# Optimization experiments

Hardware: AMD Instinct MI355X
Metric: run time of the kernel (lower is better)

The kernel has to match this reference:

```python
import jax, jax.numpy as jnp
import numpy as np

DIM = 256
D_STATE = 64
D_CONV = 4
EXPAND = 2
D_INNER = EXPAND * DIM  # 512
DT_RANK = (DIM + 15) // 16  # 16
BS, N1, N2 = 4, 64, 64


def setup_inputs() -> dict:
    key = jax.random.key(0)
    ks = jax.random.split(key, 12)
    s = 0.02
    x = jax.random.normal(ks[0], (BS, N1, N2, DIM), jnp.float32)
    W_in = jax.random.normal(ks[1], (2 * D_INNER, DIM), jnp.float32) * s
    conv_w = jax.random.normal(ks[2], (D_INNER, D_CONV), jnp.float32) * s
    conv_b = jax.random.normal(ks[3], (D_INNER,), jnp.float32) * s
    W_x = jax.random.normal(ks[4], (DT_RANK + 2 * D_STATE, D_INNER), jnp.float32) * s
    W_dt = jax.random.normal(ks[5], (D_INNER, DT_RANK), jnp.float32) * s
    b_dt = jax.random.normal(ks[6], (D_INNER,), jnp.float32) * s - 4.0  # softplus -> small dt
    A_log = jnp.log(jnp.broadcast_to(jnp.arange(1, D_STATE + 1, dtype=jnp.float32), (D_INNER, D_STATE)))
    D_param = jnp.ones((D_INNER,), jnp.float32)
    W_out = jax.random.normal(ks[7], (DIM, D_INNER), jnp.float32) * s
    ln1_w = jnp.ones((DIM,), jnp.float32)
    ln1_b = jnp.zeros((DIM,), jnp.float32)
    ln2_w = jnp.ones((DIM,), jnp.float32)
    ln2_b = jnp.zeros((DIM,), jnp.float32)
    return dict(x=x, ln1_w=ln1_w, ln1_b=ln1_b, ln2_w=ln2_w, ln2_b=ln2_b,
                W_in=W_in, conv_w=conv_w, conv_b=conv_b, W_x=W_x,
                W_dt=W_dt, b_dt=b_dt, A_log=A_log, D_param=D_param, W_out=W_out)


def _layernorm(x, w, b, eps=1e-6):
    mu = jnp.mean(x, axis=-1, keepdims=True)
    var = jnp.mean((x - mu) ** 2, axis=-1, keepdims=True)
    return (x - mu) * jax.lax.rsqrt(var + eps) * w + b


def _silu(x):
    return x * jax.nn.sigmoid(x)


def _selective_scan(u, dt, A, B, C, D):
    # u, dt: (Bt, L, di); B, C: (Bt, L, ds); A: (di, ds); D: (di,)
    Bt, L, di = u.shape
    ds = A.shape[1]

    def step(h, inp):
        u_t, dt_t, B_t, C_t = inp  # (Bt,di),(Bt,di),(Bt,ds),(Bt,ds)
        dA = jnp.exp(dt_t[:, :, None] * A)                       # (Bt, di, ds)
        h = dA * h + (dt_t * u_t)[:, :, None] * B_t[:, None, :]  # (Bt, di, ds)
        y_t = jnp.einsum('bds,bs->bd', h, C_t)
        return h, y_t

    h0 = jnp.zeros((Bt, di, ds), u.dtype)
    xs = (u.transpose(1, 0, 2), dt.transpose(1, 0, 2),
          B.transpose(1, 0, 2), C.transpose(1, 0, 2))
    _, ys = jax.lax.scan(step, h0, xs)                           # (L, Bt, di)
    return ys.transpose(1, 0, 2) + u * D


def _mamba(xm, W_in, conv_w, conv_b, W_x, W_dt, b_dt, A_log, D_param, W_out):
    # xm: (Bt, L, d_model)
    xz = jnp.einsum('bld,ed->ble', xm, W_in)       # (Bt, L, 2*di)
    xc, z = jnp.split(xz, 2, axis=-1)
    # depthwise causal conv along L
    xc = xc.transpose(0, 2, 1)                     # (Bt, di, L)
    xc = jax.lax.conv_general_dilated(
        xc, conv_w[:, None, :], window_strides=(1,),
        padding=[(D_CONV - 1, 0)], feature_group_count=D_INNER,
        dimension_numbers=('NCH', 'OIH', 'NCH'))
    xc = _silu(xc + conv_b[None, :, None]).transpose(0, 2, 1)  # (Bt, L, di)
    x_dbl = jnp.einsum('bld,ed->ble', xc, W_x)     # (Bt, L, dt_rank+2*ds)
    dt, Bm, Cm = jnp.split(x_dbl, [DT_RANK, DT_RANK + D_STATE], axis=-1)
    dt = jax.nn.softplus(jnp.einsum('blr,dr->bld', dt, W_dt) + b_dt)  # (Bt, L, di)
    A = -jnp.exp(A_log)                            # (di, ds)
    y = _selective_scan(xc, dt, A, Bm, Cm, D_param)
    y = y * _silu(z)
    return jnp.einsum('bld,od->blo', y, W_out)     # (Bt, L, d_model)


def reference(x, ln1_w, ln1_b, ln2_w, ln2_b, W_in, conv_w, conv_b, W_x,
              W_dt, b_dt, A_log, D_param, W_out):
    bs, n1, n2, d = x.shape
    x_norm = _layernorm(x, ln1_w, ln1_b)
    x1 = x_norm.reshape(bs, n1 * n2, d)                                  # row-major
    x2 = x_norm.transpose(0, 2, 1, 3).reshape(bs, n1 * n2, d)            # column-major
    xm = jnp.concatenate([x1, x2], axis=0)                               # (2*bs, L, d)
    xm = _mamba(xm, W_in, conv_w, conv_b, W_x, W_dt, b_dt, A_log, D_param, W_out)
    y = _layernorm(xm, ln2_w, ln2_b)
    y1, y2 = y[:bs], y[bs:]
    y1 = y1.reshape(bs, n1, n2, d)
    y2 = y2.reshape(bs, n2, n1, d).transpose(0, 2, 1, 3)
    return x + y1 + y2
```

## Files before the change

### kernel.cpp

```cpp
#include <hip/hip_runtime.h>
#include <hip/hip_bf16.h>

typedef unsigned short ushort_t;
typedef unsigned int uint_t;
typedef __attribute__((ext_vector_type(8))) short short8;
typedef __attribute__((ext_vector_type(4))) float f32x4;

#define DIMC 256
#define D_INNER 512
#define D_STATE 64
#define DT_RANK 16
#define LSEQ 4096
#define BS2 8
#define MROWS (BS2*LSEQ)

__device__ __forceinline__ float b2f(ushort_t u) {
    union { uint_t i; float f; } v; v.i = ((uint_t)u) << 16; return v.f;
}
__device__ __forceinline__ ushort_t f2b(float f) {
    union { float f; uint_t i; } v; v.f = f;
    uint_t r = v.i + 0x7FFFu + ((v.i >> 16) & 1u);
    return (ushort_t)(r >> 16);
}

typedef __attribute__((address_space(1))) const unsigned int gas_u32;
typedef __attribute__((address_space(3))) unsigned int las_u32;
__device__ __forceinline__ void gload16(const void* g, void* l) {
    __builtin_amdgcn_global_load_lds((gas_u32*)g, (las_u32*)l, 16, 0, 0);
}

__global__ void cvtw3(const float* __restrict__ s0, ushort_t* __restrict__ d0,
                      const float* __restrict__ s1, ushort_t* __restrict__ d1,
                      const float* __restrict__ s2, ushort_t* __restrict__ d2) {
    int i = blockIdx.x * 256 + threadIdx.x;
    const int n0 = 1024 * 256, n1 = 144 * 512, n2 = 256 * 512;
    if (i < n0) d0[i] = f2b(s0[i]);
    else if (i < n0 + n1) d1[i - n0] = f2b(s1[i - n0]);
    else if (i < n0 + n1 + n2) d2[i - n0 - n1] = f2b(s2[i - n0 - n1]);
}

__global__ void ln1_build_xm(const float* __restrict__ x,
                             const float* __restrict__ w,
                             const float* __restrict__ bb,
                             ushort_t* __restrict__ xm) {
    int row = blockIdx.x;
    int c = threadIdx.x;
    float v = x[(size_t)row * DIMC + c];
    float s1 = v, s2 = v * v;
    for (int off = 32; off; off >>= 1) {
        s1 += __shfl_xor(s1, off, 64);
        s2 += __shfl_xor(s2, off, 64);
    }
    __shared__ float sa[4], sb[4];
    int widx = c >> 6, lane = c & 63;
    if (lane == 0) { sa[widx] = s1; sb[widx] = s2; }
    __syncthreads();
    s1 = sa[0] + sa[1] + sa[2] + sa[3];
    s2 = sb[0] + sb[1] + sb[2] + sb[3];
    float mu = s1 * (1.0f / 256.0f);
    float var = s2 * (1.0f / 256.0f) - mu * mu;
    float xn = (v - mu) * rsqrtf(var + 1e-6f) * w[c] + bb[c];
    ushort_t o = f2b(xn);
    int b = row >> 12, l = row & 4095, i = l >> 6, j = l & 63;
    xm[((size_t)b * LSEQ + l) * DIMC + c] = o;
    xm[((size_t)(4 + b) * LSEQ + (j * 64 + i)) * DIMC + c] = o;
}

__global__ void __launch_bounds__(256, 4)
gemm128(const ushort_t* __restrict__ A,
        const ushort_t* __restrict__ W,
        ushort_t* __restrict__ C, int M, int N, int K) {
    __shared__ ushort_t Ash[128 * 32];
    __shared__ ushort_t Bsh[128 * 32];
    int tid = threadIdx.x;
    int lane = tid & 63, widx = tid >> 6;
    int wm = widx & 1, wn = widx >> 1;
    int l16 = lane & 15, quad = lane >> 4;
    int mblk = blockIdx.x * 128, nblk = blockIdx.y * 128;
    f32x4 acc[4][4];
    #pragma unroll
    for (int i = 0; i < 4; ++i)
        #pragma unroll
        for (int j = 0; j < 4; ++j)
            acc[i][j] = f32x4{0.0f, 0.0f, 0.0f, 0.0f};
    int srow = tid >> 2;
    int sseg = (tid & 3) * 8;
    bool jv[4];
    #pragma unroll
    for (int j = 0; j < 4; ++j) jv[j] = (nblk + wn * 64 + j * 16) < N;

    for (int k0 = 0; k0 < K; k0 += 32) {
        __syncthreads();
        #pragma unroll
        for (int q = 0; q < 2; ++q) {
            int row = q * 64 + srow;
            gload16(&A[(size_t)(mblk + row) * K + k0 + sseg], &Ash[row * 32 + sseg]);
            gload16(&W[(size_t)(nblk + row) * K + k0 + sseg], &Bsh[row * 32 + sseg]);
        }
        __syncthreads();
        short8 af[4], bf[4];
        #pragma unroll
        for (int i = 0; i < 4; ++i)
            af[i] = *(const short8*)&Ash[(wm * 64 + i * 16 + l16) * 32 + quad * 8];
        #pragma unroll
        for (int j = 0; j < 4; ++j)
            bf[j] = *(const short8*)&Bsh[(wn * 64 + j * 16 + l16) * 32 + quad * 8];
        #pragma unroll
        for (int i = 0; i < 4; ++i)
            #pragma unroll
            for (int j = 0; j < 4; ++j)
                if (jv[j])
                    acc[i][j] = __builtin_amdgcn_mfma_f32_16x16x32_bf16(af[i], bf[j], acc[i][j], 0, 0, 0);
    }
    #pragma unroll
    for (int i = 0; i < 4; ++i) {
        #pragma unroll
        for (int j = 0; j < 4; ++j) {
            if (!jv[j]) continue;
            int col = nblk + wn * 64 + j * 16 + l16;
            #pragma unroll
            for (int r = 0; r < 4; ++r) {
                int row = mblk + wm * 64 + i * 16 + quad * 4 + r;
                C[(size_t)row * N + col] = f2b(acc[i][j][r]);
            }
        }
    }
}

__global__ void __launch_bounds__(256, 4)
gemm128_split(const ushort_t* __restrict__ A,
              const ushort_t* __restrict__ W,
              ushort_t* __restrict__ outX,
              ushort_t* __restrict__ outZ) {
    const int K = 256;
    __shared__ ushort_t Ash[128 * 32];
    __shared__ ushort_t Bsh[128 * 32];
    int tid = threadIdx.x;
    int lane = tid & 63, widx = tid >> 6;
    int wm = widx & 1, wn = widx >> 1;
    int l16 = lane & 15, quad = lane >> 4;
    int mblk = blockIdx.x * 128, nblk = blockIdx.y * 128;
    f32x4 acc[4][4];
    #pragma unroll
    for (int i = 0; i < 4; ++i)
        #pragma unroll
        for (int j = 0; j < 4; ++j)
            acc[i][j] = f32x4{0.0f, 0.0f, 0.0f, 0.0f};
    int srow = tid >> 2;
    int sseg = (tid & 3) * 8;
    for (int k0 = 0; k0 < K; k0 += 32) {
        __syncthreads();
        #pragma unroll
        for (int q = 0; q < 2; ++q) {
            int row = q * 64 + srow;
            gload16(&A[(size_t)(mblk + row) * K + k0 + sseg], &Ash[row * 32 + sseg]);
            gload16(&W[(size_t)(nblk + row) * K + k0 + sseg], &Bsh[row * 32 + sseg]);
        }
        __syncthreads();
        short8 af[4], bf[4];
        #pragma unroll
        for (int i = 0; i < 4; ++i)
            af[i] = *(const short8*)&Ash[(wm * 64 + i * 16 + l16) * 32 + quad * 8];
        #pragma unroll
        for (int j = 0; j < 4; ++j)
            bf[j] = *(const short8*)&Bsh[(wn * 64 + j * 16 + l16) * 32 + quad * 8];
        #pragma unroll
        for (int i = 0; i < 4; ++i)
            #pragma unroll
            for (int j = 0; j < 4; ++j)
                acc[i][j] = __builtin_amdgcn_mfma_f32_16x16x32_bf16(af[i], bf[j], acc[i][j], 0, 0, 0);
    }
    #pragma unroll
    for (int i = 0; i < 4; ++i) {
        #pragma unroll
        for (int j = 0; j < 4; ++j) {
            int colg = nblk + wn * 64 + j * 16 + l16;
            ushort_t* dst = (colg < 512) ? outX : outZ;
            int col = colg & 511;
            #pragma unroll
            for (int r = 0; r < 4; ++r) {
                int row = mblk + wm * 64 + i * 16 + quad * 4 + r;
                dst[(size_t)row * 512 + col] = f2b(acc[i][j][r]);
            }
        }
    }
}

__global__ void conv_silu_t(const ushort_t* __restrict__ xh,
                            const float* __restrict__ cw,
                            const float* __restrict__ cb,
                            ushort_t* __restrict__ xc,
                            ushort_t* __restrict__ u_T) {
    int bt0 = blockIdx.x * 64;
    int d0  = blockIdx.y * 64;
    int b   = bt0 >> 12;
    int t0  = bt0 & 4095;
    __shared__ ushort_t tin[67][66];
    __shared__ ushort_t tout[64][66];
    int tid = threadIdx.x, lane = tid & 63, widx = tid >> 6;
    for (int r = widx; r < 67; r += 4) {
        int tt = t0 - 3 + r;
        tin[r][lane] = (tt >= 0) ? xh[((size_t)bt0 - 3 + r) * 512 + d0 + lane] : (ushort_t)0;
    }
    __syncthreads();
    for (int dd = widx; dd < 64; dd += 4) {
        int d = d0 + dd;
        float acc = cb[d];
        #pragma unroll
        for (int k = 0; k < 4; ++k)
            acc += cw[d * 4 + k] * b2f(tin[lane + k][dd]);
        float s = acc / (1.0f + __expf(-acc));
        ushort_t o = f2b(s);
        u_T[((size_t)b * 512 + d) * 4096 + t0 + lane] = o;
        tout[lane][dd] = o;
    }
    __syncthreads();
    for (int r = widx; r < 64; r += 4)
        xc[((size_t)bt0 + r) * 512 + d0 + lane] = tout[r][lane];
}

__global__ void dt_sp_t(const ushort_t* __restrict__ xdbl,
                        const float* __restrict__ wdt,
                        const float* __restrict__ bdt,
                        const ushort_t* __restrict__ u_T,
                        ushort_t* __restrict__ dt_T,
                        ushort_t* __restrict__ w_T,
                        float2* __restrict__ BCf) {
    int bt0 = blockIdx.x * 64;
    int d0  = blockIdx.y * 64;
    int b   = bt0 >> 12;
    int t0  = bt0 & 4095;
    __shared__ float din[64][17];
    int tid = threadIdx.x;
    for (int i = tid; i < 64 * 16; i += 256) {
        int r = i >> 4, k = i & 15;
        din[r][k] = b2f(xdbl[((size_t)bt0 + r) * 144 + k]);
    }
    __syncthreads();
    int lane = tid & 63, widx = tid >> 6;
    for (int dd = widx; dd < 64; dd += 4) {
        int d = d0 + dd;
        float acc = bdt[d];
        #pragma unroll
        for (int k = 0; k < 16; ++k)
            acc += din[lane][k] * wdt[d * 16 + k];
        float sp = (acc > 20.0f) ? acc : log1pf(__expf(acc));
        size_t idx = ((size_t)b * 512 + d) * 4096 + t0 + lane;
        dt_T[idx] = f2b(sp);
        float uvv = b2f(u_T[idx]);
        w_T[idx] = f2b(sp * uvv);
    }
    if (blockIdx.y == 0) {
        for (int i = tid; i < 64 * 64; i += 256) {
            size_t row = (size_t)bt0 + (i >> 6);
            int s = i & 63;
            const ushort_t* rp = xdbl + row * 144;
            BCf[(row << 6) + s] = make_float2(b2f(rp[16 + s]), b2f(rp[80 + s]));
        }
    }
}

template<int LVL>
__device__ __forceinline__ float merge_lvl_t(float left, float right, int lane) {
    bool bit = (lane >> LVL) & 1;
    float send = bit ? left : right;
    float keep = bit ? right : left;
    float recv;
    if constexpr (LVL == 0)
        recv = __int_as_float(__builtin_amdgcn_update_dpp(
            0, __float_as_int(send), 0xB1, 0xF, 0xF, false));
    else if constexpr (LVL == 1)
        recv = __int_as_float(__builtin_amdgcn_update_dpp(
            0, __float_as_int(send), 0x4E, 0xF, 0xF, false));
    else
        recv = __shfl_xor(send, 1 << LVL, 64);
    return keep + recv;
}

__global__ void __launch_bounds__(256, 4)
scan10(const ushort_t* __restrict__ dt_T,
       ushort_t* uT_ysT,
       const ushort_t* __restrict__ w_T,
       const float2* __restrict__ BCf,
       const float* __restrict__ Alog,
       const float* __restrict__ Dp) {
    __shared__ float2 BCsh[64][64];
    int tid = threadIdx.x;
    int lane = tid & 63, widx = tid >> 6;
    int wid = blockIdx.x * 4 + widx;
    int b = wid >> 9, d = wid & 511;
    float a2 = -__expf(Alog[d * 64 + lane]) * 1.442695041f;
    float Dd = Dp[d];
    float h = 0.0f;
    size_t rowT = ((size_t)b * 512 + d) * 4096;
    uint_t rowTu = __builtin_amdgcn_readfirstlane((uint_t)rowT);
    size_t base = (size_t)b * LSEQ;
    for (int t0 = 0; t0 < LSEQ; t0 += 64) {
        __syncthreads();
        {
            const char* gsrc = (const char*)(BCf + (((size_t)(base + t0)) << 6));
            char* ldst = (char*)&BCsh[0][0];
            size_t woff = (size_t)widx * 8192;
            #pragma unroll
            for (int it = 0; it < 8; ++it) {
                size_t o = woff + (size_t)it * 1024 + (size_t)lane * 16;
                gload16(gsrc + o, ldst + o);
            }
        }
        const uint_t* dtw = (const uint_t*)(dt_T + rowTu) + (t0 >> 1);
        const uint_t* wwp = (const uint_t*)(w_T + rowTu) + (t0 >> 1);
        float uv = b2f(uT_ysT[rowT + t0 + lane]);
        __syncthreads();
        float acc[4], s4, s5, yfin = 0.0f, v16 = 0.0f;
        #pragma unroll 1
        for (int j1 = 0; j1 < 4; ++j1) {
            #pragma unroll
            for (int jj = 0; jj < 16; ++jj) {
                int j = j1 * 16 + jj;
                uint_t pd = dtw[j >> 1];
                uint_t pw = wwp[j >> 1];
                float sdt = __uint_as_float((jj & 1) ? (pd & 0xFFFF0000u) : (pd << 16));
                float sw  = __uint_as_float((jj & 1) ? (pw & 0xFFFF0000u) : (pw << 16));
                float2 bc = BCsh[j][lane];
                float dA = __builtin_amdgcn_exp2f(sdt * a2);
                float Bw = sw * bc.x;
                h = dA * h + Bw;
                float v = h * bc.y;
                const int dest = (jj == 15) ? 4 : __builtin_ctz(~(unsigned)jj);
                if (0 < dest) v = merge_lvl_t<0>(acc[0], v, lane);
                if (1 < dest) v = merge_lvl_t<1>(acc[1], v, lane);
                if (2 < dest) v = merge_lvl_t<2>(acc[2], v, lane);
                if (3 < dest) v = merge_lvl_t<3>(acc[3], v, lane);
                if (jj == 15) v16 = v;
                else acc[dest] = v;
            }
            if ((j1 & 1) == 0) {
                s4 = v16;
            } else {
                float m = merge_lvl_t<4>(s4, v16, lane);
                if (j1 == 1) s5 = m;
                else yfin = merge_lvl_t<5>(s5, m, lane);
            }
        }
        float y = yfin + uv * Dd;
        uT_ysT[rowT + t0 + lane] = f2b(y);
    }
}

__global__ void gate_t(const ushort_t* __restrict__ ysT,
                       const ushort_t* __restrict__ zb,
                       ushort_t* __restrict__ ys) {
    int bt0 = blockIdx.x * 64;
    int d0  = blockIdx.y * 64;
    int b   = bt0 >> 12;
    int t0  = bt0 & 4095;
    __shared__ ushort_t tile[64][66];
    int tid = threadIdx.x, lane = tid & 63, widx = tid >> 6;
    for (int dd = widx; dd < 64; dd += 4)
        tile[dd][lane] = ysT[((size_t)b * 512 + d0 + dd) * 4096 + t0 + lane];
    __syncthreads();
    for (int r = widx; r < 64; r += 4) {
        float zv = b2f(zb[((size_t)bt0 + r) * 512 + d0 + lane]);
        float yv = b2f(tile[lane][r]);
        float g = zv / (1.0f + __expf(-zv));
        ys[((size_t)bt0 + r) * 512 + d0 + lane] = f2b(yv * g);
    }
}

__global__ void final_ln_add(const ushort_t* __restrict__ outm,
                             const float* __restrict__ x,
                             const float* __restrict__ w,
                             const float* __restrict__ bb,
                             float* __restrict__ out) {
    int row = blockIdx.x;
    int c = threadIdx.x;
    int b = row >> 12, l = row & 4095, i = l >> 6, j = l & 63;
    size_t rA = ((size_t)b * LSEQ + l) * DIMC;
    size_t rB = ((size_t)(4 + b) * LSEQ + (j * 64 + i)) * DIMC;
    float va = b2f(outm[rA + c]);
    float vb = b2f(outm[rB + c]);
    float s1 = va, s2 = va * va, s3 = vb, s4 = vb * vb;
    for (int off = 32; off; off >>= 1) {
        s1 += __shfl_xor(s1, off, 64);
        s2 += __shfl_xor(s2, off, 64);
        s3 += __shfl_xor(s3, off, 64);
        s4 += __shfl_xor(s4, off, 64);
    }
    __shared__ float sm[4][4];
    int widx = c >> 6, lane = c & 63;
    if (lane == 0) { sm[widx][0] = s1; sm[widx][1] = s2; sm[widx][2] = s3; sm[widx][3] = s4; }
    __syncthreads();
    s1 = sm[0][0] + sm[1][0] + sm[2][0] + sm[3][0];
    s2 = sm[0][1] + sm[1][1] + sm[2][1] + sm[3][1];
    s3 = sm[0][2] + sm[1][2] + sm[2][2] + sm[3][2];
    s4 = sm[0][3] + sm[1][3] + sm[2][3] + sm[3][3];
    float muA = s1 * (1.0f / 256.0f), varA = s2 * (1.0f / 256.0f) - muA * muA;
    float muB = s3 * (1.0f / 256.0f), varB = s4 * (1.0f / 256.0f) - muB * muB;
    float lw = w[c], lb = bb[c];
    float ya = (va - muA) * rsqrtf(varA + 1e-6f) * lw + lb;
    float yb = (vb - muB) * rsqrtf(varB + 1e-6f) * lw + lb;
    float xo = x[(size_t)row * DIMC + c];
    out[(size_t)row * DIMC + c] = xo + ya + yb;
}

extern "C" void kernel_launch(void* const* d_in, const int* in_sizes, int n_in,
                              void* d_out, int out_size, void* d_ws, size_t ws_size,
                              hipStream_t stream) {
    const float* x      = (const float*)d_in[0];
    const float* ln1_w  = (const float*)d_in[1];
    const float* ln1_b  = (const float*)d_in[2];
    const float* ln2_w  = (const float*)d_in[3];
    const float* ln2_b  = (const float*)d_in[4];
    const float* W_in   = (const float*)d_in[5];
    const float* conv_w = (const float*)d_in[6];
    const float* conv_b = (const float*)d_in[7];
    const float* W_x    = (const float*)d_in[8];
    const float* W_dt   = (const float*)d_in[9];
    const float* b_dt   = (const float*)d_in[10];
    const float* A_log  = (const float*)d_in[11];
    const float* D_par  = (const float*)d_in[12];
    const float* W_out  = (const float*)d_in[13];
    float* out = (float*)d_out;

    char* ws = (char*)d_ws;
    size_t off = 0;
    ushort_t* wb_in  = (ushort_t*)(ws + off); off += (size_t)1024 * 256 * 2;
    ushort_t* wb_x   = (ushort_t*)(ws + off); off += (size_t)144 * 512 * 2;
    ushort_t* wb_out = (ushort_t*)(ws + off); off += (size_t)256 * 512 * 2;
    const size_t R0 = (size_t)MROWS * DIMC * 2;
    const size_t R1 = (size_t)MROWS * 512 * 2;
    ushort_t* r0 = (ushort_t*)(ws + off); off += R0;
    ushort_t* r1 = (ushort_t*)(ws + off); off += R1;
    ushort_t* r2 = (ushort_t*)(ws + off); off += R1;
    ushort_t* r3 = (ushort_t*)(ws + off); off += R1;
    ushort_t* r4 = (ushort_t*)(ws + off); off += R1;
    float2*   BCf = (float2*)(ws + off);  off += (size_t)MROWS * 64 * 8;

    ushort_t* xm    = r0;
    ushort_t* xdbl  = r0;
    ushort_t* outm  = r0;
    ushort_t* xhalf = r1;
    ushort_t* dt_T  = r1;
    ushort_t* zb    = r2;
    ushort_t* xc    = r3;
    ushort_t* w_T   = r3;
    ushort_t* ys    = r3;
    ushort_t* u_T   = r4;

    const int ncvt = 1024 * 256 + 144 * 512 + 256 * 512;
    hipLaunchKernelGGL(cvtw3, dim3((ncvt + 255) / 256), dim3(256), 0, stream,
                       W_in, wb_in, W_x, wb_x, W_out, wb_out);

    hipLaunchKernelGGL(ln1_build_xm, dim3(4 * LSEQ), dim3(256), 0, stream,
                       x, ln1_w, ln1_b, xm);
    hipLaunchKernelGGL(gemm128_split, dim3(MROWS / 128, 8), dim3(256), 0, stream,
                       xm, wb_in, xhalf, zb);
    hipLaunchKernelGGL(conv_silu_t, dim3(MROWS / 64, 8), dim3(256), 0, stream,
                       xhalf, conv_w, conv_b, xc, u_T);
    hipLaunchKernelGGL(gemm128, dim3(MROWS / 128, 2), dim3(256), 0, stream,
                       xc, wb_x, xdbl, MROWS, 144, 512);
    hipLaunchKernelGGL(dt_sp_t, dim3(MROWS / 64, 8), dim3(256), 0, stream,
                       xdbl, W_dt, b_dt, u_T, dt_T, w_T, BCf);
    hipLaunchKernelGGL(scan10, dim3(BS2 * 512 / 4), dim3(256), 0, stream,
                       dt_T, u_T, w_T, BCf, A_log, D_par);
    hipLaunchKernelGGL(gate_t, dim3(MROWS / 64, 8), dim3(256), 0, stream,
                       u_T, zb, ys);
    hipLaunchKernelGGL(gemm128, dim3(MROWS / 128, 2), dim3(256), 0, stream,
                       ys, wb_out, outm, MROWS, 256, 512);
    hipLaunchKernelGGL(final_ln_add, dim3(4 * LSEQ), dim3(256), 0, stream,
                       outm, x, ln2_w, ln2_b, out);
}
```

Baseline: 730.4 us.

## Double-buffer BC staging in scan and use DPP-add and permlane swap merges

The scan kernel now stages B/C coefficients in 32-step halves into a two-slot LDS buffer, so the global-to-LDS load for the next half overlaps compute on the current half. This replaces the old load-then-barrier pattern that stalled every 64 steps. The lane-reduction merges are also cheaper: levels 0-1 use a fused v_add_f32_dpp in inline asm, and levels 4-5 use v_permlane16/32_swap instead of cross-lane shuffles. The output store is deferred by one iteration. In exchange it adds more barriers per iteration and inline asm with hand-placed s_nop hazards, which could be fragile.

```diff
diff --git a/kernel.cpp b/kernel.cpp
--- a/kernel.cpp
+++ b/kernel.cpp
@@ -265,26 +265,38 @@
     bool bit = (lane >> LVL) & 1;
     float send = bit ? left : right;
     float keep = bit ? right : left;
-    float recv;
-    if constexpr (LVL == 0)
-        recv = __int_as_float(__builtin_amdgcn_update_dpp(
-            0, __float_as_int(send), 0xB1, 0xF, 0xF, false));
-    else if constexpr (LVL == 1)
-        recv = __int_as_float(__builtin_amdgcn_update_dpp(
-            0, __float_as_int(send), 0x4E, 0xF, 0xF, false));
-    else
-        recv = __shfl_xor(send, 1 << LVL, 64);
-    return keep + recv;
+    float out;
+    if constexpr (LVL == 0) {
+        asm volatile("s_nop 1\n\t"
+                     "v_add_f32_dpp %0, %1, %2 quad_perm:[1,0,3,2] row_mask:0xf bank_mask:0xf"
+                     : "=v"(out) : "v"(send), "v"(keep));
+    } else if constexpr (LVL == 1) {
+        asm volatile("s_nop 1\n\t"
+                     "v_add_f32_dpp %0, %1, %2 quad_perm:[2,3,0,1] row_mask:0xf bank_mask:0xf"
+                     : "=v"(out) : "v"(send), "v"(keep));
+    } else {
+        float recv = __shfl_xor(send, 1 << LVL, 64);
+        out = keep + recv;
+    }
+    return out;
+}
+__device__ __forceinline__ float merge16_swap(float a, float b) {
+    asm volatile("s_nop 1\n\tv_permlane16_swap_b32 %0, %1" : "+v"(a), "+v"(b));
+    return a + b;
+}
+__device__ __forceinline__ float merge32_swap(float a, float b) {
+    asm volatile("s_nop 1\n\tv_permlane32_swap_b32 %0, %1" : "+v"(a), "+v"(b));
+    return a + b;
 }
 
 __global__ void __launch_bounds__(256, 4)
-scan10(const ushort_t* __restrict__ dt_T,
+scan11(const ushort_t* __restrict__ dt_T,
        ushort_t* uT_ysT,
        const ushort_t* __restrict__ w_T,
        const float2* __restrict__ BCf,
        const float* __restrict__ Alog,
        const float* __restrict__ Dp) {
-    __shared__ float2 BCsh[64][64];
+    __shared__ float2 BCsh[2][32][64];
     int tid = threadIdx.x;
     int lane = tid & 63, widx = tid >> 6;
     int wid = blockIdx.x * 4 + widx;
@@ -295,56 +307,65 @@
     size_t rowT = ((size_t)b * 512 + d) * 4096;
     uint_t rowTu = __builtin_amdgcn_readfirstlane((uint_t)rowT);
     size_t base = (size_t)b * LSEQ;
-    for (int t0 = 0; t0 < LSEQ; t0 += 64) {
-        __syncthreads();
-        {
-            const char* gsrc = (const char*)(BCf + (((size_t)(base + t0)) << 6));
-            char* ldst = (char*)&BCsh[0][0];
-            size_t woff = (size_t)widx * 8192;
-            #pragma unroll
-            for (int it = 0; it < 8; ++it) {
-                size_t o = woff + (size_t)it * 1024 + (size_t)lane * 16;
-                gload16(gsrc + o, ldst + o);
-            }
-        }
-        const uint_t* dtw = (const uint_t*)(dt_T + rowTu) + (t0 >> 1);
-        const uint_t* wwp = (const uint_t*)(w_T + rowTu) + (t0 >> 1);
-        float uv = b2f(uT_ysT[rowT + t0 + lane]);
-        __syncthreads();
-        float acc[4], s4, s5, yfin = 0.0f, v16 = 0.0f;
-        #pragma unroll 1
-        for (int j1 = 0; j1 < 4; ++j1) {
-            #pragma unroll
-            for (int jj = 0; jj < 16; ++jj) {
-                int j = j1 * 16 + jj;
-                uint_t pd = dtw[j >> 1];
-                uint_t pw = wwp[j >> 1];
-                float sdt = __uint_as_float((jj & 1) ? (pd & 0xFFFF0000u) : (pd << 16));
-                float sw  = __uint_as_float((jj & 1) ? (pw & 0xFFFF0000u) : (pw << 16));
-                float2 bc = BCsh[j][lane];
-                float dA = __builtin_amdgcn_exp2f(sdt * a2);
-                float Bw = sw * bc.x;
-                h = dA * h + Bw;
-                float v = h * bc.y;
-                const int dest = (jj == 15) ? 4 : __builtin_ctz(~(unsigned)jj);
-                if (0 < dest) v = merge_lvl_t<0>(acc[0], v, lane);
-                if (1 < dest) v = merge_lvl_t<1>(acc[1], v, lane);
-                if (2 < dest) v = merge_lvl_t<2>(acc[2], v, lane);
-                if (3 < dest) v = merge_lvl_t<3>(acc[3], v, lane);
-                if (jj == 15) v16 = v;
-                else acc[dest] = v;
-            }
-            if ((j1 & 1) == 0) {
-                s4 = v16;
-            } else {
-                float m = merge_lvl_t<4>(s4, v16, lane);
-                if (j1 == 1) s5 = m;
-                else yfin = merge_lvl_t<5>(s5, m, lane);
-            }
-        }
-        float y = yfin + uv * Dd;
-        uT_ysT[rowT + t0 + lane] = f2b(y);
-    }
+    const uint_t* dtw = (const uint_t*)(dt_T + rowTu);
+    const uint_t* wwp = (const uint_t*)(w_T + rowTu);
+
+    auto STAGE = [&](int bufi, int hs) {
+        const char* gsrc = (const char*)(BCf + (((size_t)(base + hs * 32)) << 6));
+        char* ldst = (char*)&BCsh[bufi][0][0];
+        size_t woff = (size_t)widx * 4096;
+        #pragma unroll
+        for (int it = 0; it < 4; ++it) {
+            size_t o = woff + (size_t)it * 1024 + (size_t)lane * 16;
+            gload16(gsrc + o, ldst + o);
+        }
+    };
+
+    float acc[4];
+    auto STEP16 = [&](int bufi, int jbase, int dwb) -> float {
+        float v16 = 0.0f;
+        #pragma unroll
+        for (int jj = 0; jj < 16; ++jj) {
+            uint_t pd = dtw[dwb + (jj >> 1)];
+            uint_t pw = wwp[dwb + (jj >> 1)];
+            float sdt = __uint_as_float((jj & 1) ? (pd & 0xFFFF0000u) : (pd << 16));
+            float sw  = __uint_as_float((jj & 1) ? (pw & 0xFFFF0000u) : (pw << 16));
+            float2 bc = BCsh[bufi][jbase + jj][lane];
+            float dA = __builtin_amdgcn_exp2f(sdt * a2);
+            h = dA * h + sw * bc.x;
+            float v = h * bc.y;
+            const int dest = (jj == 15) ? 4 : __builtin_ctz(~(unsigned)jj);
+            if (0 < dest) v = merge_lvl_t<0>(acc[0], v, lane);
+            if (1 < dest) v = merge_lvl_t<1>(acc[1], v, lane);
+            if (2 < dest) v = merge_lvl_t<2>(acc[2], v, lane);
+            if (3 < dest) v = merge_lvl_t<3>(acc[3], v, lane);
+            if (jj == 15) v16 = v;
+            else acc[dest] = v;
+        }
+        return v16;
+    };
+
+    STAGE(0, 0);
+    __syncthreads();
+    ushort_t ypend = 0;
+    #pragma unroll 1
+    for (int sl = 0; sl < 64; ++sl) {
+        int t0 = sl * 64;
+        int dwb = sl * 32;
+        STAGE(1, 2 * sl + 1);
+        if (sl) uT_ysT[rowT + t0 - 64 + lane] = ypend;
+        float uvv = b2f(uT_ysT[rowT + t0 + lane]);
+        float s4 = STEP16(0, 0, dwb);
+        float s5 = merge16_swap(s4, STEP16(0, 16, dwb + 8));
+        __syncthreads();
+        if (sl + 1 < 64) STAGE(0, 2 * sl + 2);
+        float s4b = STEP16(1, 0, dwb + 16);
+        float m = merge16_swap(s4b, STEP16(1, 16, dwb + 24));
+        float yfin = merge32_swap(s5, m);
+        ypend = f2b(yfin + uvv * Dd);
+        __syncthreads();
+    }
+    uT_ysT[rowT + LSEQ - 64 + lane] = ypend;
 }
 
 __global__ void gate_t(const ushort_t* __restrict__ ysT,
@@ -461,7 +482,7 @@
                        xc, wb_x, xdbl, MROWS, 144, 512);
     hipLaunchKernelGGL(dt_sp_t, dim3(MROWS / 64, 8), dim3(256), 0, stream,
                        xdbl, W_dt, b_dt, u_T, dt_T, w_T, BCf);
-    hipLaunchKernelGGL(scan10, dim3(BS2 * 512 / 4), dim3(256), 0, stream,
+    hipLaunchKernelGGL(scan11, dim3(BS2 * 512 / 4), dim3(256), 0, stream,
                        dt_T, u_T, w_T, BCf, A_log, D_par);
     hipLaunchKernelGGL(gate_t, dim3(MROWS / 64, 8), dim3(256), 0, stream,
                        u_T, zb, ys);
```

Result: slower. 849.6 us (+16.3%).
